# Kernel tuning notes

Hardware: AMD Instinct MI355X
Metric: run time of the kernel (lower is better)

Reference implementation:

```python
import jax, jax.numpy as jnp
import numpy as np

EPS = 1e-8  # torch.cosine_similarity eps
TEMPERATURE = 1.0


def setup_inputs() -> dict:
    key = jax.random.key(0)
    ks = jax.random.split(key, 12)
    B = 16384
    inp = {
        "user_ids": jax.random.randint(ks[0], (B, 8), 0, 100000),
        "item_ids": jax.random.randint(ks[1], (B, 4), 0, 50000),
        "sample_weight": jax.random.uniform(ks[2], (B,), jnp.float32, 0.01, 1.0),
        "user_table": jax.random.normal(ks[3], (100000, 64), jnp.float32) * 0.05,
        "item_table": jax.random.normal(ks[4], (50000, 64), jnp.float32) * 0.05,
        "uW1": jax.random.normal(ks[5], (512, 256), jnp.float32) * 0.04,
        "ub1": jnp.zeros((256,), jnp.float32),
        "uW2": jax.random.normal(ks[6], (256, 128), jnp.float32) * 0.06,
        "ub2": jnp.zeros((128,), jnp.float32),
        "iW1": jax.random.normal(ks[7], (256, 256), jnp.float32) * 0.06,
        "ib1": jnp.zeros((256,), jnp.float32),
        "iW2": jax.random.normal(ks[8], (256, 128), jnp.float32) * 0.06,
        "ib2": jnp.zeros((128,), jnp.float32),
        "n_neg": 3,
    }
    return inp


def _tower(ids, table, W1, b1, W2, b2):
    # embedding lookup [B, F, D] -> concat -> [B, F*D], then 2-layer relu MLP
    B = ids.shape[0]
    e = table[ids].reshape(B, -1)
    h = jax.nn.relu(e @ W1 + b1)
    return jax.nn.relu(h @ W2 + b2)


def reference(user_ids, item_ids, sample_weight, user_table, item_table,
              uW1, ub1, uW2, ub2, iW1, ib1, iW2, ib2, n_neg):
    u = _tower(user_ids, user_table, uW1, ub1, uW2, ub2)  # [B, 128]
    v = _tower(item_ids, item_table, iW1, ib1, iW2, ib2)  # [B, 128]
    # cosine similarity per row (torch eps clamp on norms)
    un = jnp.maximum(jnp.linalg.norm(u, axis=1), EPS)
    vn = jnp.maximum(jnp.linalg.norm(v, axis=1), EPS)
    y = jnp.sum(u * v, axis=1) / (un * vn)
    # sampling-bias correction
    y = y - jnp.log(sample_weight)
    # vectorized wrap-around in-batch negative gather:
    # scores[i] = [y[i], y[(i+1)%B], ..., y[(i+n_neg)%B]]
    B = y.shape[0]
    idx = (jnp.arange(B)[:, None] + jnp.arange(n_neg + 1)[None, :]) % B
    scores = y[idx] / TEMPERATURE  # [B, 1+n_neg]
    return scores
```

## Files before the change

### kernel.cpp

```cpp
#include <hip/hip_runtime.h>
#include <math.h>

#define CEPS 1e-8f

typedef __attribute__((ext_vector_type(8))) short bf16x8;
typedef __attribute__((ext_vector_type(4))) float f32x4;
typedef __attribute__((ext_vector_type(4))) unsigned int u32x4;

__device__ __forceinline__ unsigned short f2bf(float f) {
    unsigned u = __builtin_bit_cast(unsigned, f);
    u += 0x7fffu + ((u >> 16) & 1u);
    return (unsigned short)(u >> 16);
}

__global__ __launch_bounds__(256)
void pack_all(const float* __restrict__ uW1, const float* __restrict__ uW2,
              const float* __restrict__ iW1, const float* __restrict__ iW2,
              unsigned short* __restrict__ o1, unsigned short* __restrict__ o2,
              unsigned short* __restrict__ o3, unsigned short* __restrict__ o4)
{
    int g = blockIdx.x * 256 + threadIdx.x;
    const float* src; unsigned short* dst; int N; int base;
    if (g < 16384)      { src = uW1; dst = o1; N = 256; base = 0;     }
    else if (g < 20480) { src = uW2; dst = o2; N = 128; base = 16384; }
    else if (g < 28672) { src = iW1; dst = o3; N = 256; base = 20480; }
    else                { src = iW2; dst = o4; N = 128; base = 28672; }
    int i = g - base;
    int kg = i / N, n = i - kg * N;
    unsigned short tmp[8];
    #pragma unroll
    for (int j = 0; j < 8; ++j)
        tmp[j] = f2bf(src[(kg * 8 + j) * N + n]);
    *reinterpret_cast<bf16x8*>(dst + ((size_t)i << 3)) =
        *reinterpret_cast<bf16x8*>(tmp);
}


template<int F>
__device__ __forceinline__ void stage_emb(const int* __restrict__ ids,
                                          const float* __restrict__ table,
                                          unsigned short* e_s, int row0, int tid)
{
    constexpr int FC = F * 8;
    constexpr int IT = F / 2;
    int idv[IT];
    #pragma unroll
    for (int it = 0; it < IT; ++it) {
        int c = tid + it * 512;
        int r = c / FC, f = (c % FC) >> 3;
        idv[it] = ids[(row0 + r) * F + f];
    }
    #pragma unroll
    for (int it = 0; it < IT; ++it) {
        int c = tid + it * 512;
        int r = c / FC, rem = c % FC, ci = rem & 7;
        const float* src = table + (size_t)idv[it] * 64 + ci * 8;
        float4 aa = *reinterpret_cast<const float4*>(src);
        float4 bb = *reinterpret_cast<const float4*>(src + 4);
        u32x4 pk;
        pk.x = f2bf(aa.x) | ((unsigned)f2bf(aa.y) << 16);
        pk.y = f2bf(aa.z) | ((unsigned)f2bf(aa.w) << 16);
        pk.z = f2bf(bb.x) | ((unsigned)f2bf(bb.y) << 16);
        pk.w = f2bf(bb.z) | ((unsigned)f2bf(bb.w) << 16);
        int byte = r * (F * 128) + rem * 16;
        byte ^= (r & 7) << 4;
        *reinterpret_cast<u32x4*>(reinterpret_cast<char*>(e_s) + byte) = pk;
    }
}

template<int K1>
__device__ __forceinline__ bf16x8 loadA(const unsigned short* e_s, int ks, int m,
                                        int l15, int l4)
{
    int row = m * 16 + l15;
    int byte = row * (K1 * 2) + ks * 64 + l4 * 16;
    byte ^= (row & 7) << 4;
    return *reinterpret_cast<const bf16x8*>(
               reinterpret_cast<const char*>(e_s) + byte);
}

template<int NFRAG>
__device__ __forceinline__ void preloadB(const unsigned short* __restrict__ Wp,
                                         int N, int colbase, int lane, bf16x8* b0)
{
    const unsigned short* base =
        Wp + ((((lane >> 4) * N) + colbase + (lane & 15)) << 3);
    #pragma unroll
    for (int n = 0; n < NFRAG; ++n)
        b0[n] = *reinterpret_cast<const bf16x8*>(base + (n << 7));
}

template<int K1>
__device__ __forceinline__ void gemm1(
    const unsigned short* e_s, unsigned short* h_s,
    const unsigned short* __restrict__ W1p, const float* __restrict__ b1,
    int lane, int w, const bf16x8* b0)
{
    constexpr int NKS = K1 / 32;
    const int l15 = lane & 15, l4 = lane >> 4;
    const int colbase = w * 32;
    f32x4 acc[2][2];
    #pragma unroll
    for (int m = 0; m < 2; ++m)
        #pragma unroll
        for (int n = 0; n < 2; ++n) acc[m][n] = (f32x4){0.f, 0.f, 0.f, 0.f};

    const unsigned short* Wbase = W1p + (((l4 * 256) + colbase + l15) << 3);
    bf16x8 aB[2][2], bB[2][2];
    bB[0][0] = b0[0];
    bB[0][1] = b0[1];
    #pragma unroll
    for (int m = 0; m < 2; ++m) aB[0][m] = loadA<K1>(e_s, 0, m, l15, l4);

    #pragma unroll
    for (int ks = 0; ks < NKS; ++ks) {
        const int cur = ks & 1, nxt = cur ^ 1;
        if (ks + 1 < NKS) {
            #pragma unroll
            for (int m = 0; m < 2; ++m)
                aB[nxt][m] = loadA<K1>(e_s, ks + 1, m, l15, l4);
            #pragma unroll
            for (int n = 0; n < 2; ++n)
                bB[nxt][n] = *reinterpret_cast<const bf16x8*>(
                                 Wbase + (ks + 1) * 8192 + (n << 7));
        }
        #pragma unroll
        for (int n = 0; n < 2; ++n)
            #pragma unroll
            for (int m = 0; m < 2; ++m)
                acc[m][n] = __builtin_amdgcn_mfma_f32_16x16x32_bf16(
                                aB[cur][m], bB[cur][n], acc[m][n], 0, 0, 0);
    }
    #pragma unroll
    for (int n = 0; n < 2; ++n) {
        int col = colbase + n * 16 + l15;
        float bias = b1[col];
        #pragma unroll
        for (int m = 0; m < 2; ++m)
            #pragma unroll
            for (int r = 0; r < 4; ++r) {
                int row = m * 16 + l4 * 4 + r;
                float v = acc[m][n][r] + bias;
                v = v > 0.f ? v : 0.f;
                int byte = (row * 256 + col) * 2;
                byte ^= (row & 7) << 4;
                *reinterpret_cast<unsigned short*>(
                    reinterpret_cast<char*>(h_s) + byte) = f2bf(v);
            }
    }
}

__device__ __forceinline__ void gemm2(
    const unsigned short* h_s, const unsigned short* __restrict__ W2p,
    f32x4 (&acc)[2], int lane, int w, bf16x8 b0)
{
    const int l15 = lane & 15, l4 = lane >> 4;
    const int col = w * 16 + l15;
    #pragma unroll
    for (int m = 0; m < 2; ++m) acc[m] = (f32x4){0.f, 0.f, 0.f, 0.f};

    const unsigned short* Wbase = W2p + (((l4 * 128) + col) << 3);
    bf16x8 aB[2][2], bB[2];
    bB[0] = b0;
    #pragma unroll
    for (int m = 0; m < 2; ++m) aB[0][m] = loadA<256>(h_s, 0, m, l15, l4);

    #pragma unroll
    for (int ks = 0; ks < 8; ++ks) {
        const int cur = ks & 1, nxt = cur ^ 1;
        if (ks + 1 < 8) {
            #pragma unroll
            for (int m = 0; m < 2; ++m)
                aB[nxt][m] = loadA<256>(h_s, ks + 1, m, l15, l4);
            bB[nxt] = *reinterpret_cast<const bf16x8*>(Wbase + (ks + 1) * 4096);
        }
        #pragma unroll
        for (int m = 0; m < 2; ++m)
            acc[m] = __builtin_amdgcn_mfma_f32_16x16x32_bf16(
                         aB[cur][m], bB[cur], acc[m], 0, 0, 0);
    }
}

__global__ __launch_bounds__(512, 4)
void fused_sbc(const int* __restrict__ user_ids,  const int* __restrict__ item_ids,
               const float* __restrict__ user_table, const float* __restrict__ item_table,
               const unsigned short* __restrict__ uW1p, const float* __restrict__ ub1,
               const unsigned short* __restrict__ uW2p, const float* __restrict__ ub2,
               const unsigned short* __restrict__ iW1p, const float* __restrict__ ib1,
               const unsigned short* __restrict__ iW2p, const float* __restrict__ ib2,
               const float* __restrict__ sw, float* __restrict__ out,
               int B, int nn1)
{
    __shared__ unsigned short e_s[32 * 512];
    __shared__ unsigned short h_s[32 * 256];
    __shared__ float red[8][32][3];

    const int tid  = threadIdx.x;
    const int lane = tid & 63;
    const int w    = tid >> 6;
    const int row0 = blockIdx.x * 32;

    bf16x8 b0u1[2];
    preloadB<2>(uW1p, 256, w * 32, lane, b0u1);
    stage_emb<8>(user_ids, user_table, e_s, row0, tid);
    __syncthreads();

    gemm1<512>(e_s, h_s, uW1p, ub1, lane, w, b0u1);
    bf16x8 b0u2[1], b0i1[2];
    preloadB<1>(uW2p, 128, w * 16, lane, b0u2);
    preloadB<2>(iW1p, 256, w * 32, lane, b0i1);
    __syncthreads();

    stage_emb<4>(item_ids, item_table, e_s, row0, tid);
    f32x4 accU[2];
    gemm2(h_s, uW2p, accU, lane, w, b0u2[0]);
    __syncthreads();

    gemm1<256>(e_s, h_s, iW1p, ib1, lane, w, b0i1);
    bf16x8 b0i2[1];
    preloadB<1>(iW2p, 128, w * 16, lane, b0i2);
    __syncthreads();

    f32x4 accV[2];
    gemm2(h_s, iW2p, accV, lane, w, b0i2[0]);

    const int l15 = lane & 15, l4 = lane >> 4;
    const int col = w * 16 + l15;
    const float bu = ub2[col];
    const float bv = ib2[col];
    float pd[8], pu[8], pv[8];
    #pragma unroll
    for (int m = 0; m < 2; ++m)
        #pragma unroll
        for (int r = 0; r < 4; ++r) {
            float uval = accU[m][r] + bu;
            float vval = accV[m][r] + bv;
            uval = uval > 0.f ? uval : 0.f;
            vval = vval > 0.f ? vval : 0.f;
            int i = m * 4 + r;
            pd[i] = uval * vval;
            pu[i] = uval * uval;
            pv[i] = vval * vval;
        }
    #pragma unroll
    for (int off = 1; off < 16; off <<= 1) {
        #pragma unroll
        for (int i = 0; i < 8; ++i) {
            pd[i] += __shfl_xor(pd[i], off);
            pu[i] += __shfl_xor(pu[i], off);
            pv[i] += __shfl_xor(pv[i], off);
        }
    }
    if (l15 == 0) {
        #pragma unroll
        for (int m = 0; m < 2; ++m)
            #pragma unroll
            for (int r = 0; r < 4; ++r) {
                int row = m * 16 + l4 * 4 + r;
                int i = m * 4 + r;
                red[w][row][0] = pd[i];
                red[w][row][1] = pu[i];
                red[w][row][2] = pv[i];
            }
    }
    __syncthreads();

    if (tid < 32) {
        int row = tid;
        float d = 0.f, su = 0.f, sv = 0.f;
        #pragma unroll
        for (int ww = 0; ww < 8; ++ww) {
            d  += red[ww][row][0];
            su += red[ww][row][1];
            sv += red[ww][row][2];
        }
        float un = fmaxf(sqrtf(su), CEPS);
        float vn = fmaxf(sqrtf(sv), CEPS);
        int grow = row0 + row;
        float yv = d / (un * vn) - logf(sw[grow]);
        for (int j = 0; j < nn1; ++j) {
            int idx = grow - j;
            if (idx < 0) idx += B;
            out[idx * nn1 + j] = yv;
        }
    }
}

extern "C" void kernel_launch(void* const* d_in, const int* in_sizes, int n_in,
                              void* d_out, int out_size, void* d_ws, size_t ws_size,
                              hipStream_t stream)
{
    const int*   user_ids   = (const int*)  d_in[0];
    const int*   item_ids   = (const int*)  d_in[1];
    const float* sw         = (const float*)d_in[2];
    const float* user_table = (const float*)d_in[3];
    const float* item_table = (const float*)d_in[4];
    const float* uW1        = (const float*)d_in[5];
    const float* ub1        = (const float*)d_in[6];
    const float* uW2        = (const float*)d_in[7];
    const float* ub2        = (const float*)d_in[8];
    const float* iW1        = (const float*)d_in[9];
    const float* ib1        = (const float*)d_in[10];
    const float* iW2        = (const float*)d_in[11];
    const float* ib2        = (const float*)d_in[12];

    const int B   = in_sizes[2];
    const int nn1 = out_size / B;

    unsigned short* wp   = (unsigned short*)d_ws;
    unsigned short* uW1p = wp;
    unsigned short* uW2p = wp + 131072;
    unsigned short* iW1p = wp + 163840;
    unsigned short* iW2p = wp + 229376;
    float* out = (float*)d_out;

    pack_all<<<128, 256, 0, stream>>>(uW1, uW2, iW1, iW2,
                                      uW1p, uW2p, iW1p, iW2p);
    fused_sbc<<<B / 32, 512, 0, stream>>>(user_ids, item_ids,
                                          user_table, item_table,
                                          uW1p, ub1, uW2p, ub2,
                                          iW1p, ib1, iW2p, ib2,
                                          sw, out, B, nn1);
}
```

Baseline: 33.95 us.

## Double block rows to 64 with 1024 threads and separate user/item embedding buffers

New measurement: 33.57 us. Within noise of the previous version (-1.1%).

```diff
diff --git a/kernel.cpp b/kernel.cpp
--- a/kernel.cpp
+++ b/kernel.cpp
@@ -42,17 +42,17 @@
                                           unsigned short* e_s, int row0, int tid)
 {
     constexpr int FC = F * 8;
-    constexpr int IT = F / 2;
+    constexpr int IT = (64 * FC) / 1024;
     int idv[IT];
     #pragma unroll
     for (int it = 0; it < IT; ++it) {
-        int c = tid + it * 512;
+        int c = tid + it * 1024;
         int r = c / FC, f = (c % FC) >> 3;
         idv[it] = ids[(row0 + r) * F + f];
     }
     #pragma unroll
     for (int it = 0; it < IT; ++it) {
-        int c = tid + it * 512;
+        int c = tid + it * 1024;
         int r = c / FC, rem = c % FC, ci = rem & 7;
         const float* src = table + (size_t)idv[it] * 64 + ci * 8;
         float4 aa = *reinterpret_cast<const float4*>(src);
@@ -68,94 +68,70 @@
     }
 }
 
-template<int K1>
-__device__ __forceinline__ bf16x8 loadA(const unsigned short* e_s, int ks, int m,
-                                        int l15, int l4)
-{
-    int row = m * 16 + l15;
-    int byte = row * (K1 * 2) + ks * 64 + l4 * 16;
+template<int KB>
+__device__ __forceinline__ bf16x8 loadA(const unsigned short* s, int rowbase,
+                                        int ks, int m, int l15, int l4)
+{
+    int row = rowbase + m * 16 + l15;
+    int byte = row * (KB * 2) + ks * 64 + l4 * 16;
     byte ^= (row & 7) << 4;
     return *reinterpret_cast<const bf16x8*>(
-               reinterpret_cast<const char*>(e_s) + byte);
-}
-
-template<int NFRAG>
-__device__ __forceinline__ void preloadB(const unsigned short* __restrict__ Wp,
-                                         int N, int colbase, int lane, bf16x8* b0)
-{
-    const unsigned short* base =
-        Wp + ((((lane >> 4) * N) + colbase + (lane & 15)) << 3);
-    #pragma unroll
-    for (int n = 0; n < NFRAG; ++n)
-        b0[n] = *reinterpret_cast<const bf16x8*>(base + (n << 7));
+               reinterpret_cast<const char*>(s) + byte);
 }
 
 template<int K1>
 __device__ __forceinline__ void gemm1(
     const unsigned short* e_s, unsigned short* h_s,
     const unsigned short* __restrict__ W1p, const float* __restrict__ b1,
-    int lane, int w, const bf16x8* b0)
+    int l15, int l4, int w, bf16x8 b0)
 {
     constexpr int NKS = K1 / 32;
-    const int l15 = lane & 15, l4 = lane >> 4;
-    const int colbase = w * 32;
-    f32x4 acc[2][2];
-    #pragma unroll
-    for (int m = 0; m < 2; ++m)
-        #pragma unroll
-        for (int n = 0; n < 2; ++n) acc[m][n] = (f32x4){0.f, 0.f, 0.f, 0.f};
-
-    const unsigned short* Wbase = W1p + (((l4 * 256) + colbase + l15) << 3);
-    bf16x8 aB[2][2], bB[2][2];
-    bB[0][0] = b0[0];
-    bB[0][1] = b0[1];
-    #pragma unroll
-    for (int m = 0; m < 2; ++m) aB[0][m] = loadA<K1>(e_s, 0, m, l15, l4);
+    const int col = w * 16 + l15;
+    f32x4 acc[4];
+    #pragma unroll
+    for (int m = 0; m < 4; ++m) acc[m] = (f32x4){0.f, 0.f, 0.f, 0.f};
+
+    const unsigned short* Wbase = W1p + (((l4 * 256) + col) << 3);
+    bf16x8 aB[2][4], bB[2];
+    bB[0] = b0;
+    #pragma unroll
+    for (int m = 0; m < 4; ++m) aB[0][m] = loadA<K1>(e_s, 0, 0, m, l15, l4);
 
     #pragma unroll
     for (int ks = 0; ks < NKS; ++ks) {
         const int cur = ks & 1, nxt = cur ^ 1;
         if (ks + 1 < NKS) {
             #pragma unroll
-            for (int m = 0; m < 2; ++m)
-                aB[nxt][m] = loadA<K1>(e_s, ks + 1, m, l15, l4);
-            #pragma unroll
-            for (int n = 0; n < 2; ++n)
-                bB[nxt][n] = *reinterpret_cast<const bf16x8*>(
-                                 Wbase + (ks + 1) * 8192 + (n << 7));
-        }
-        #pragma unroll
-        for (int n = 0; n < 2; ++n)
-            #pragma unroll
-            for (int m = 0; m < 2; ++m)
-                acc[m][n] = __builtin_amdgcn_mfma_f32_16x16x32_bf16(
-                                aB[cur][m], bB[cur][n], acc[m][n], 0, 0, 0);
-    }
-    #pragma unroll
-    for (int n = 0; n < 2; ++n) {
-        int col = colbase + n * 16 + l15;
-        float bias = b1[col];
-        #pragma unroll
-        for (int m = 0; m < 2; ++m)
-            #pragma unroll
-            for (int r = 0; r < 4; ++r) {
-                int row = m * 16 + l4 * 4 + r;
-                float v = acc[m][n][r] + bias;
-                v = v > 0.f ? v : 0.f;
-                int byte = (row * 256 + col) * 2;
-                byte ^= (row & 7) << 4;
-                *reinterpret_cast<unsigned short*>(
-                    reinterpret_cast<char*>(h_s) + byte) = f2bf(v);
-            }
-    }
+            for (int m = 0; m < 4; ++m)
+                aB[nxt][m] = loadA<K1>(e_s, 0, ks + 1, m, l15, l4);
+            bB[nxt] = *reinterpret_cast<const bf16x8*>(Wbase + (ks + 1) * 8192);
+        }
+        #pragma unroll
+        for (int m = 0; m < 4; ++m)
+            acc[m] = __builtin_amdgcn_mfma_f32_16x16x32_bf16(
+                         aB[cur][m], bB[cur], acc[m], 0, 0, 0);
+    }
+    const float bias = b1[col];
+    #pragma unroll
+    for (int m = 0; m < 4; ++m)
+        #pragma unroll
+        for (int r = 0; r < 4; ++r) {
+            int row = m * 16 + l4 * 4 + r;
+            float v = acc[m][r] + bias;
+            v = v > 0.f ? v : 0.f;
+            int byte = (row * 256 + col) * 2;
+            byte ^= (row & 7) << 4;
+            *reinterpret_cast<unsigned short*>(
+                reinterpret_cast<char*>(h_s) + byte) = f2bf(v);
+        }
 }
 
 __device__ __forceinline__ void gemm2(
     const unsigned short* h_s, const unsigned short* __restrict__ W2p,
-    f32x4 (&acc)[2], int lane, int w, bf16x8 b0)
-{
-    const int l15 = lane & 15, l4 = lane >> 4;
-    const int col = w * 16 + l15;
+    f32x4 (&acc)[2], int l15, int l4, int w, bf16x8 b0)
+{
+    const int col = (w & 7) * 16 + l15;
+    const int rowbase = (w >> 3) * 32;
     #pragma unroll
     for (int m = 0; m < 2; ++m) acc[m] = (f32x4){0.f, 0.f, 0.f, 0.f};
 
@@ -163,7 +139,7 @@
     bf16x8 aB[2][2], bB[2];
     bB[0] = b0;
     #pragma unroll
-    for (int m = 0; m < 2; ++m) aB[0][m] = loadA<256>(h_s, 0, m, l15, l4);
+    for (int m = 0; m < 2; ++m) aB[0][m] = loadA<256>(h_s, rowbase, 0, m, l15, l4);
 
     #pragma unroll
     for (int ks = 0; ks < 8; ++ks) {
@@ -171,7 +147,7 @@
         if (ks + 1 < 8) {
             #pragma unroll
             for (int m = 0; m < 2; ++m)
-                aB[nxt][m] = loadA<256>(h_s, ks + 1, m, l15, l4);
+                aB[nxt][m] = loadA<256>(h_s, rowbase, ks + 1, m, l15, l4);
             bB[nxt] = *reinterpret_cast<const bf16x8*>(Wbase + (ks + 1) * 4096);
         }
         #pragma unroll
@@ -181,7 +157,7 @@
     }
 }
 
-__global__ __launch_bounds__(512, 4)
+__global__ __launch_bounds__(1024, 4)
 void fused_sbc(const int* __restrict__ user_ids,  const int* __restrict__ item_ids,
                const float* __restrict__ user_table, const float* __restrict__ item_table,
                const unsigned short* __restrict__ uW1p, const float* __restrict__ ub1,
@@ -191,41 +167,43 @@
                const float* __restrict__ sw, float* __restrict__ out,
                int B, int nn1)
 {
-    __shared__ unsigned short e_s[32 * 512];
-    __shared__ unsigned short h_s[32 * 256];
-    __shared__ float red[8][32][3];
+    __shared__ unsigned short e_u[64 * 512];
+    __shared__ unsigned short e_i[64 * 256];
+    __shared__ unsigned short h_s[64 * 256];
+    __shared__ float red[8][64][3];
 
     const int tid  = threadIdx.x;
     const int lane = tid & 63;
     const int w    = tid >> 6;
-    const int row0 = blockIdx.x * 32;
-
-    bf16x8 b0u1[2];
-    preloadB<2>(uW1p, 256, w * 32, lane, b0u1);
-    stage_emb<8>(user_ids, user_table, e_s, row0, tid);
-    __syncthreads();
-
-    gemm1<512>(e_s, h_s, uW1p, ub1, lane, w, b0u1);
-    bf16x8 b0u2[1], b0i1[2];
-    preloadB<1>(uW2p, 128, w * 16, lane, b0u2);
-    preloadB<2>(iW1p, 256, w * 32, lane, b0i1);
-    __syncthreads();
-
-    stage_emb<4>(item_ids, item_table, e_s, row0, tid);
+    const int l15  = lane & 15, l4 = lane >> 4;
+    const int row0 = blockIdx.x * 64;
+
+    bf16x8 b0u1 = *reinterpret_cast<const bf16x8*>(
+                      uW1p + ((l4 * 256 + w * 16 + l15) << 3));
+    stage_emb<8>(user_ids, user_table, e_u, row0, tid);
+    stage_emb<4>(item_ids, item_table, e_i, row0, tid);
+    __syncthreads();
+
+    gemm1<512>(e_u, h_s, uW1p, ub1, l15, l4, w, b0u1);
+    bf16x8 b0u2 = *reinterpret_cast<const bf16x8*>(
+                      uW2p + ((l4 * 128 + (w & 7) * 16 + l15) << 3));
+    bf16x8 b0i1 = *reinterpret_cast<const bf16x8*>(
+                      iW1p + ((l4 * 256 + w * 16 + l15) << 3));
+    __syncthreads();
+
     f32x4 accU[2];
-    gemm2(h_s, uW2p, accU, lane, w, b0u2[0]);
-    __syncthreads();
-
-    gemm1<256>(e_s, h_s, iW1p, ib1, lane, w, b0i1);
-    bf16x8 b0i2[1];
-    preloadB<1>(iW2p, 128, w * 16, lane, b0i2);
+    gemm2(h_s, uW2p, accU, l15, l4, w, b0u2);
+    __syncthreads();
+
+    gemm1<256>(e_i, h_s, iW1p, ib1, l15, l4, w, b0i1);
+    bf16x8 b0i2 = *reinterpret_cast<const bf16x8*>(
+                      iW2p + ((l4 * 128 + (w & 7) * 16 + l15) << 3));
     __syncthreads();
 
     f32x4 accV[2];
-    gemm2(h_s, iW2p, accV, lane, w, b0i2[0]);
-
-    const int l15 = lane & 15, l4 = lane >> 4;
-    const int col = w * 16 + l15;
+    gemm2(h_s, iW2p, accV, l15, l4, w, b0i2);
+
+    const int col = (w & 7) * 16 + l15;
     const float bu = ub2[col];
     const float bv = ib2[col];
     float pd[8], pu[8], pv[8];
@@ -252,27 +230,28 @@
         }
     }
     if (l15 == 0) {
+        const int rowbase = (w >> 3) * 32;
         #pragma unroll
         for (int m = 0; m < 2; ++m)
             #pragma unroll
             for (int r = 0; r < 4; ++r) {
-                int row = m * 16 + l4 * 4 + r;
+                int row = rowbase + m * 16 + l4 * 4 + r;
                 int i = m * 4 + r;
-                red[w][row][0] = pd[i];
-                red[w][row][1] = pu[i];
-                red[w][row][2] = pv[i];
+                red[w & 7][row][0] = pd[i];
+                red[w & 7][row][1] = pu[i];
+                red[w & 7][row][2] = pv[i];
             }
     }
     __syncthreads();
 
-    if (tid < 32) {
+    if (tid < 64) {
         int row = tid;
         float d = 0.f, su = 0.f, sv = 0.f;
         #pragma unroll
-        for (int ww = 0; ww < 8; ++ww) {
-            d  += red[ww][row][0];
-            su += red[ww][row][1];
-            sv += red[ww][row][2];
+        for (int cg = 0; cg < 8; ++cg) {
+            d  += red[cg][row][0];
+            su += red[cg][row][1];
+            sv += red[cg][row][2];
         }
         float un = fmaxf(sqrtf(su), CEPS);
         float vn = fmaxf(sqrtf(sv), CEPS);
@@ -316,9 +295,9 @@
 
     pack_all<<<128, 256, 0, stream>>>(uW1, uW2, iW1, iW2,
                                       uW1p, uW2p, iW1p, iW2p);
-    fused_sbc<<<B / 32, 512, 0, stream>>>(user_ids, item_ids,
-                                          user_table, item_table,
-                                          uW1p, ub1, uW2p, ub2,
-                                          iW1p, ib1, iW2p, ib2,
-                                          sw, out, B, nn1);
-}
+    fused_sbc<<<B / 64, 1024, 0, stream>>>(user_ids, item_ids,
+                                           user_table, item_table,
+                                           uW1p, ub1, uW2p, ub2,
+                                           iW1p, ib1, iW2p, ib2,
+                                           sw, out, B, nn1);
+}
```
